# Optimization experiments

Measured on AMD Instinct MI355X. Metric: run time of the kernel, lower is better.

## Reference

```python
import jax, jax.numpy as jnp
import numpy as np

NU, NI, D, E = 200_000, 100_000, 128, 600_000
EPS = 1e-5


def _linear(x, W, b):
    # torch nn.Linear: y = x @ W.T + b, W is [out, in]
    return x @ W.T + b


def _layer_norm(x, g, b):
    mu = jnp.mean(x, axis=-1, keepdims=True)
    var = jnp.mean((x - mu) ** 2, axis=-1, keepdims=True)
    return (x - mu) * jax.lax.rsqrt(var + EPS) * g + b


def _sym_norm_w(row, col, n_src, n_dst):
    ones = jnp.ones(row.shape, jnp.float32)
    deg_s = jax.ops.segment_sum(ones, row, num_segments=n_src)
    deg_d = jax.ops.segment_sum(ones, col, num_segments=n_dst)
    inv_s = jnp.where(deg_s > 0, deg_s ** -0.5, 0.0)
    inv_d = jnp.where(deg_d > 0, deg_d ** -0.5, 0.0)
    return inv_s[row] * inv_d[col]  # [E]


def _relation(x_src, row, col, n_dst, Wl, bl, Wf, bf):
    w = _sym_norm_w(row, col, x_src.shape[0], n_dst)
    m = x_src[row] * w[:, None]                      # gather + scale, [E, D]
    s = jax.ops.segment_sum(m, col, num_segments=n_dst)      # sum messages
    sq = jax.ops.segment_sum(m * m, col, num_segments=n_dst)  # sum of squares
    fm = 0.5 * (s * s - sq)                          # FM interaction
    return _linear(s, Wl, bl) + _linear(fm, Wf, bf)


def setup_inputs() -> dict:
    key = jax.random.key(0)
    ks = jax.random.split(key, 24)
    scale = 1.0 / np.sqrt(D)
    p = lambda k: jax.random.normal(k, (D, D), jnp.float32) * scale
    return {
        "h_user": jax.random.normal(ks[0], (NU, D), jnp.float32),
        "h_item": jax.random.normal(ks[1], (NI, D), jnp.float32),
        "ei_u2i_src": jax.random.randint(ks[2], (E,), 0, NU),
        "ei_u2i_dst": jax.random.randint(ks[3], (E,), 0, NI),
        "ei_i2u_src": jax.random.randint(ks[4], (E,), 0, NI),
        "ei_i2u_dst": jax.random.randint(ks[5], (E,), 0, NU),
        "Ws_user": p(ks[6]), "bs_user": jnp.zeros((D,), jnp.float32),
        "Ws_item": p(ks[7]), "bs_item": jnp.zeros((D,), jnp.float32),
        "Wlin_u2i": p(ks[8]), "blin_u2i": jnp.zeros((D,), jnp.float32),
        "Wfm_u2i": p(ks[9]), "bfm_u2i": jnp.zeros((D,), jnp.float32),
        "Wlin_i2u": p(ks[10]), "blin_i2u": jnp.zeros((D,), jnp.float32),
        "Wfm_i2u": p(ks[11]), "bfm_i2u": jnp.zeros((D,), jnp.float32),
        "g_user": jnp.ones((D,), jnp.float32), "be_user": jnp.zeros((D,), jnp.float32),
        "g_item": jnp.ones((D,), jnp.float32), "be_item": jnp.zeros((D,), jnp.float32),
    }


def reference(h_user, h_item, ei_u2i_src, ei_u2i_dst, ei_i2u_src, ei_i2u_dst,
              Ws_user, bs_user, Ws_item, bs_item,
              Wlin_u2i, blin_u2i, Wfm_u2i, bfm_u2i,
              Wlin_i2u, blin_i2u, Wfm_i2u, bfm_i2u,
              g_user, be_user, g_item, be_item):
    out_u = _linear(h_user, Ws_user, bs_user)
    out_i = _linear(h_item, Ws_item, bs_item)
    # edge type (user, rates, item): src=user, dst=item
    out_i = out_i + _relation(h_user, ei_u2i_src, ei_u2i_dst, NI,
                              Wlin_u2i, blin_u2i, Wfm_u2i, bfm_u2i)
    # edge type (item, rated_by, user): src=item, dst=user
    out_u = out_u + _relation(h_item, ei_i2u_src, ei_i2u_dst, NU,
                              Wlin_i2u, blin_i2u, Wfm_i2u, bfm_i2u)
    out_u = jax.nn.relu(_layer_norm(out_u, g_user, be_user))
    out_i = jax.nn.relu(_layer_norm(out_i, g_item, be_item))
    return out_u, out_i
```

## Files before the change

kernel.cpp:

```cpp
#include <hip/hip_runtime.h>
#include <hip/hip_bf16.h>

#define NU 200000
#define NI 100000
#define DD 128
#define EE 600000
#define CAP 28
#define NXCD 8
#define ZINT (NI + NU + NXCD * NU + NXCD * NI)
#define ZN4 (ZINT / 4)
#define ZB  ((ZN4 + 255) / 256)
#define NW8 (6 * DD * DD / 8)
#define NWB ((NW8 + 255) / 256)
#define NPB2 ((2 * EE + 255) / 256)
#define NIV ((NU + NI + 255) / 256)
#define NSC (((NU + NI) * 16 + 255) / 256)
#define NGAB ((NI + 3) / 4)
#define NGBB ((NU + 3) / 4)
#define NMA ((NI + 127) / 128)
#define NMB ((NU + 127) / 128)

typedef __attribute__((ext_vector_type(8))) short bf16x8;
typedef __attribute__((ext_vector_type(4))) float f32x4;

__device__ __forceinline__ unsigned short f2bf(float f) {
    unsigned int u = __float_as_uint(f);
    u += 0x7fff + ((u >> 16) & 1);
    return (unsigned short)(u >> 16);
}
__device__ __forceinline__ float bf2f(unsigned short h) {
    return __uint_as_float(((unsigned int)h) << 16);
}
__device__ __forceinline__ int xcc_id() {
    unsigned x;
    asm volatile("s_getreg_b32 %0, hwreg(HW_REG_XCC_ID)" : "=s"(x));
    return (int)(x & 7);
}
__device__ __forceinline__ void atomic_inc_l2(int* p) {
    __hip_atomic_fetch_add(p, 1, __ATOMIC_RELAXED, __HIP_MEMORY_SCOPE_WORKGROUP);
}

__global__ void prep_kernel(int* __restrict__ z,
                            const float* __restrict__ w0, const float* __restrict__ w1,
                            const float* __restrict__ w2, const float* __restrict__ w3,
                            const float* __restrict__ w4, const float* __restrict__ w5,
                            unsigned short* __restrict__ wb) {
    int b = blockIdx.x;
    if (b < ZB) {
        int i = b * 256 + threadIdx.x;
        if (i < ZN4) ((int4*)z)[i] = make_int4(0, 0, 0, 0);
        return;
    }
    int i = (b - ZB) * 256 + threadIdx.x;
    if (i >= NW8) return;
    int wsel = i >> 11;
    int k = i & 2047;
    const float* src = (wsel == 0) ? w0 : (wsel == 1) ? w1 : (wsel == 2) ? w2
                     : (wsel == 3) ? w3 : (wsel == 4) ? w4 : w5;
    const float4* p = (const float4*)src + (size_t)k * 2;
    float4 v0 = p[0], v1 = p[1];
    union { unsigned short us[8]; uint4 u4; } r;
    r.us[0] = f2bf(v0.x); r.us[1] = f2bf(v0.y); r.us[2] = f2bf(v0.z); r.us[3] = f2bf(v0.w);
    r.us[4] = f2bf(v1.x); r.us[5] = f2bf(v1.y); r.us[6] = f2bf(v1.z); r.us[7] = f2bf(v1.w);
    ((uint4*)(wb + wsel * DD * DD))[k] = r.u4;
}

__global__ __launch_bounds__(256) void place2_kernel(
        const int* __restrict__ srcA, const int* __restrict__ dstA,
        const int* __restrict__ srcB, const int* __restrict__ dstB,
        int* __restrict__ degAs_p, int* __restrict__ cntA, int* __restrict__ bktA,
        int* __restrict__ degBs_p, int* __restrict__ cntB, int* __restrict__ bktB) {
    int e = blockIdx.x * 256 + threadIdx.x;
    if (e >= 2 * EE) return;
    int xcc = xcc_id();
    if (e < EE) {
        int r = srcA[e], c = dstA[e];
        atomic_inc_l2(&degAs_p[xcc * NU + r]);
        int slot = atomicAdd(&cntA[c], 1);
        if (slot < CAP) bktA[c * CAP + slot] = r;
    } else {
        int f = e - EE;
        int r = srcB[f], c = dstB[f];
        atomic_inc_l2(&degBs_p[xcc * NI + r]);
        int slot = atomicAdd(&cntB[c], 1);
        if (slot < CAP) bktB[c * CAP + slot] = r;
    }
}

__global__ void invmerge_kernel(const int* __restrict__ degAs_p,
                                const int* __restrict__ degBs_p,
                                float* __restrict__ invAs, float* __restrict__ invBs) {
    int i = blockIdx.x * 256 + threadIdx.x;
    if (i < NU) {
        int d = 0;
        #pragma unroll
        for (int x = 0; x < NXCD; ++x) d += degAs_p[x * NU + i];
        invAs[i] = (d > 0) ? rsqrtf((float)d) : 0.f;
    } else if (i < NU + NI) {
        int j = i - NU;
        int d = 0;
        #pragma unroll
        for (int x = 0; x < NXCD; ++x) d += degBs_p[x * NI + j];
        invBs[j] = (d > 0) ? rsqrtf((float)d) : 0.f;
    }
}

__global__ void scaleconv_kernel(const float* __restrict__ h_user,
                                 const float* __restrict__ h_item,
                                 const float* __restrict__ invAs,
                                 const float* __restrict__ invBs,
                                 unsigned short* __restrict__ hubS,
                                 unsigned short* __restrict__ hibS) {
    int i = blockIdx.x * 256 + threadIdx.x;
    const float* h; const float* inv; unsigned short* out; int row, k8;
    if (i < NU * 16) { h = h_user; inv = invAs; out = hubS; row = i >> 4; k8 = (i & 15) * 8; }
    else {
        int j = i - NU * 16;
        if (j >= NI * 16) return;
        h = h_item; inv = invBs; out = hibS; row = j >> 4; k8 = (j & 15) * 8;
    }
    float w = inv[row];
    const float4* p = (const float4*)(h + (size_t)row * DD + k8);
    float4 v0 = p[0], v1 = p[1];
    union { unsigned short us[8]; uint4 u4; } r;
    r.us[0] = f2bf(v0.x * w); r.us[1] = f2bf(v0.y * w);
    r.us[2] = f2bf(v0.z * w); r.us[3] = f2bf(v0.w * w);
    r.us[4] = f2bf(v1.x * w); r.us[5] = f2bf(v1.y * w);
    r.us[6] = f2bf(v1.z * w); r.us[7] = f2bf(v1.w * w);
    *(uint4*)(out + (size_t)row * DD + k8) = r.u4;
}

__device__ __forceinline__ void gather_rows(const unsigned short* __restrict__ xS,
                                            const int* __restrict__ cnt,
                                            const int* __restrict__ bkt,
                                            unsigned short* __restrict__ sOut,
                                            unsigned short* __restrict__ fmOut,
                                            int N, int bid) {
    int d = bid * 4 + (threadIdx.x >> 6);
    int lane = threadIdx.x & 63;
    if (d >= N) return;
    int cfull = cnt[d];
    float invD = (cfull > 0) ? rsqrtf((float)cfull) : 0.f;
    float invD2 = invD * invD;
    int dg = min(cfull, CAP);
    const int* brow = bkt + (size_t)d * CAP;
    float s0 = 0.f, s1 = 0.f, q0 = 0.f, q1 = 0.f;
    for (int j = 0; j < dg; j += 4) {
        int rem = dg - j;
        int4 iv = *(const int4*)(brow + j);
        int i0 = iv.x;
        int i1 = (rem > 1) ? iv.y : i0;
        int i2 = (rem > 2) ? iv.z : i0;
        int i3 = (rem > 3) ? iv.w : i0;
        unsigned int u0 = *(const unsigned int*)(xS + (size_t)i0 * DD + lane * 2);
        unsigned int u1 = *(const unsigned int*)(xS + (size_t)i1 * DD + lane * 2);
        unsigned int u2 = *(const unsigned int*)(xS + (size_t)i2 * DD + lane * 2);
        unsigned int u3 = *(const unsigned int*)(xS + (size_t)i3 * DD + lane * 2);
        u1 = (rem > 1) ? u1 : 0u;
        u2 = (rem > 2) ? u2 : 0u;
        u3 = (rem > 3) ? u3 : 0u;
        float a, b;
        a = bf2f((unsigned short)(u0 & 0xffff)); b = bf2f((unsigned short)(u0 >> 16));
        s0 += a; q0 += a * a; s1 += b; q1 += b * b;
        a = bf2f((unsigned short)(u1 & 0xffff)); b = bf2f((unsigned short)(u1 >> 16));
        s0 += a; q0 += a * a; s1 += b; q1 += b * b;
        a = bf2f((unsigned short)(u2 & 0xffff)); b = bf2f((unsigned short)(u2 >> 16));
        s0 += a; q0 += a * a; s1 += b; q1 += b * b;
        a = bf2f((unsigned short)(u3 & 0xffff)); b = bf2f((unsigned short)(u3 >> 16));
        s0 += a; q0 += a * a; s1 += b; q1 += b * b;
    }
    float ss0 = s0 * invD, ss1 = s1 * invD;
    float f0 = 0.5f * (ss0 * ss0 - q0 * invD2);
    float f1 = 0.5f * (ss1 * ss1 - q1 * invD2);
    unsigned int spack = (unsigned int)f2bf(ss0) | ((unsigned int)f2bf(ss1) << 16);
    unsigned int fpack = (unsigned int)f2bf(f0) | ((unsigned int)f2bf(f1) << 16);
    *(unsigned int*)(sOut  + (size_t)d * DD + lane * 2) = spack;
    *(unsigned int*)(fmOut + (size_t)d * DD + lane * 2) = fpack;
}

__global__ __launch_bounds__(256) void gather2_kernel(
        const unsigned short* __restrict__ hubS, const unsigned short* __restrict__ hibS,
        const int* __restrict__ cntA, const int* __restrict__ bktA,
        const int* __restrict__ cntB, const int* __restrict__ bktB,
        unsigned short* __restrict__ sbA, unsigned short* __restrict__ fbA,
        unsigned short* __restrict__ sbB, unsigned short* __restrict__ fbB) {
    int b = blockIdx.x;
    if (b < NGAB) {
        gather_rows(hubS, cntA, bktA, sbA, fbA, NI, b);
    } else {
        gather_rows(hibS, cntB, bktB, sbB, fbB, NU, b - NGAB);
    }
}

__device__ __forceinline__ bf16x8 a_from_f32(const float* __restrict__ X, size_t off) {
    float4 lo = *(const float4*)(X + off);
    float4 hi = *(const float4*)(X + off + 4);
    union { unsigned short us[8]; bf16x8 v; } r;
    r.us[0] = f2bf(lo.x); r.us[1] = f2bf(lo.y); r.us[2] = f2bf(lo.z); r.us[3] = f2bf(lo.w);
    r.us[4] = f2bf(hi.x); r.us[5] = f2bf(hi.y); r.us[6] = f2bf(hi.z); r.us[7] = f2bf(hi.w);
    return r.v;
}

__device__ __forceinline__ void gemm_ln_block(unsigned char* Wlds, int bid,
        const float* __restrict__ Xh32,
        const unsigned short* __restrict__ Xs, const unsigned short* __restrict__ Xf,
        const unsigned short* __restrict__ W0, const unsigned short* __restrict__ W1,
        const unsigned short* __restrict__ W2,
        const float* __restrict__ B0, const float* __restrict__ B1,
        const float* __restrict__ B2,
        const float* __restrict__ g, const float* __restrict__ be,
        float* __restrict__ out, int N) {
    int tid  = threadIdx.x;
    int wv   = tid >> 6, lane = tid & 63;
    int rlo  = lane & 15, kg = lane >> 4;
    int rowbase = bid * 128 + wv * 32;
    int ar0 = min(rowbase + rlo,      N - 1);
    int ar1 = min(rowbase + 16 + rlo, N - 1);

    f32x4 acc[2][8];
    #pragma unroll
    for (int rt = 0; rt < 2; ++rt)
        #pragma unroll
        for (int jt = 0; jt < 8; ++jt) acc[rt][jt] = (f32x4){0.f, 0.f, 0.f, 0.f};

    const unsigned short* Wp[3] = {W0, W1, W2};
    size_t a0off = (size_t)ar0 * DD + kg * 8;
    size_t a1off = (size_t)ar1 * DD + kg * 8;
    #pragma unroll
    for (int s3 = 0; s3 < 3; ++s3) {
        const uint4* Wg = (const uint4*)Wp[s3];
        #pragma unroll
        for (int it = 0; it < 8; ++it) {
            int slot = it * 256 + tid;
            int row = slot >> 4, c = slot & 15;
            uint4 v = Wg[slot];
            int sc = c ^ (row & 7);
            *(uint4*)(Wlds + ((row << 8) + (sc << 4))) = v;
        }
        __syncthreads();
        #pragma unroll
        for (int ks = 0; ks < 4; ++ks) {
            bf16x8 bfr[8];
            #pragma unroll
            for (int jt = 0; jt < 8; ++jt) {
                int jrow = jt * 16 + rlo;
                int boff = (jrow << 8) + ((((ks << 2) + kg) ^ (jrow & 7)) << 4);
                bfr[jt] = *(const bf16x8*)(Wlds + boff);
            }
            bf16x8 a0, a1;
            if (s3 == 0) {
                a0 = a_from_f32(Xh32, a0off + ks * 32);
                a1 = a_from_f32(Xh32, a1off + ks * 32);
            } else {
                const unsigned short* X = (s3 == 1) ? Xs : Xf;
                a0 = *(const bf16x8*)(X + a0off + ks * 32);
                a1 = *(const bf16x8*)(X + a1off + ks * 32);
            }
            #pragma unroll
            for (int jt = 0; jt < 8; ++jt)
                acc[0][jt] = __builtin_amdgcn_mfma_f32_16x16x32_bf16(a0, bfr[jt], acc[0][jt], 0, 0, 0);
            #pragma unroll
            for (int jt = 0; jt < 8; ++jt)
                acc[1][jt] = __builtin_amdgcn_mfma_f32_16x16x32_bf16(a1, bfr[jt], acc[1][jt], 0, 0, 0);
        }
        __syncthreads();
    }

    float bsum[8], gg[8], bb[8];
    #pragma unroll
    for (int jt = 0; jt < 8; ++jt) {
        int col = jt * 16 + rlo;
        bsum[jt] = B0[col] + B1[col] + B2[col];
        gg[jt] = g[col]; bb[jt] = be[col];
    }
    #pragma unroll
    for (int rt = 0; rt < 2; ++rt) {
        float s1[4] = {0.f, 0.f, 0.f, 0.f}, s2[4] = {0.f, 0.f, 0.f, 0.f};
        #pragma unroll
        for (int jt = 0; jt < 8; ++jt)
            #pragma unroll
            for (int r = 0; r < 4; ++r) {
                float v = acc[rt][jt][r] + bsum[jt];
                acc[rt][jt][r] = v;
                s1[r] += v;
                s2[r] += v * v;
            }
        #pragma unroll
        for (int m = 1; m < 16; m <<= 1)
            #pragma unroll
            for (int r = 0; r < 4; ++r) {
                s1[r] += __shfl_xor(s1[r], m);
                s2[r] += __shfl_xor(s2[r], m);
            }
        #pragma unroll
        for (int r = 0; r < 4; ++r) {
            int grow = rowbase + rt * 16 + kg * 4 + r;
            if (grow >= N) continue;
            float mu  = s1[r] * (1.f / 128.f);
            float var = s2[r] * (1.f / 128.f) - mu * mu;
            float inv = rsqrtf(var + 1e-5f);
            #pragma unroll
            for (int jt = 0; jt < 8; ++jt) {
                int col = jt * 16 + rlo;
                float o = (acc[rt][jt][r] - mu) * inv * gg[jt] + bb[jt];
                out[(size_t)grow * DD + col] = fmaxf(o, 0.f);
            }
        }
    }
}

__global__ __launch_bounds__(256) void gemm2_kernel(
        const float* __restrict__ h_user, const float* __restrict__ h_item,
        const unsigned short* __restrict__ sbA, const unsigned short* __restrict__ fbA,
        const unsigned short* __restrict__ sbB, const unsigned short* __restrict__ fbB,
        const unsigned short* __restrict__ WsU, const unsigned short* __restrict__ WsI,
        const unsigned short* __restrict__ WlA, const unsigned short* __restrict__ WfA,
        const unsigned short* __restrict__ WlB, const unsigned short* __restrict__ WfB,
        const float* __restrict__ bs_user, const float* __restrict__ bs_item,
        const float* __restrict__ blA, const float* __restrict__ bfA,
        const float* __restrict__ blB, const float* __restrict__ bfB,
        const float* __restrict__ g_user, const float* __restrict__ be_user,
        const float* __restrict__ g_item, const float* __restrict__ be_item,
        float* __restrict__ out_u, float* __restrict__ out_i) {
    __shared__ __align__(16) unsigned char Wlds[32768];
    int b = blockIdx.x;
    if (b < NMA) {
        gemm_ln_block(Wlds, b, h_item, sbA, fbA, WsI, WlA, WfA,
                      bs_item, blA, bfA, g_item, be_item, out_i, NI);
    } else {
        gemm_ln_block(Wlds, b - NMA, h_user, sbB, fbB, WsU, WlB, WfB,
                      bs_user, blB, bfB, g_user, be_user, out_u, NU);
    }
}

extern "C" void kernel_launch(void* const* d_in, const int* in_sizes, int n_in,
                              void* d_out, int out_size, void* d_ws, size_t ws_size,
                              hipStream_t stream) {
    const float* h_user   = (const float*)d_in[0];
    const float* h_item   = (const float*)d_in[1];
    const int*   u2i_src  = (const int*)d_in[2];
    const int*   u2i_dst  = (const int*)d_in[3];
    const int*   i2u_src  = (const int*)d_in[4];
    const int*   i2u_dst  = (const int*)d_in[5];
    const float* Ws_user  = (const float*)d_in[6];
    const float* bs_user  = (const float*)d_in[7];
    const float* Ws_item  = (const float*)d_in[8];
    const float* bs_item  = (const float*)d_in[9];
    const float* Wlin_u2i = (const float*)d_in[10];
    const float* blin_u2i = (const float*)d_in[11];
    const float* Wfm_u2i  = (const float*)d_in[12];
    const float* bfm_u2i  = (const float*)d_in[13];
    const float* Wlin_i2u = (const float*)d_in[14];
    const float* blin_i2u = (const float*)d_in[15];
    const float* Wfm_i2u  = (const float*)d_in[16];
    const float* bfm_i2u  = (const float*)d_in[17];
    const float* g_user   = (const float*)d_in[18];
    const float* be_user  = (const float*)d_in[19];
    const float* g_item   = (const float*)d_in[20];
    const float* be_item  = (const float*)d_in[21];

    float* out   = (float*)d_out;
    float* out_u = out;
    float* out_i = out + (size_t)NU * DD;

    char* wsb = (char*)d_ws;
    int* cntA    = (int*)wsb;     wsb += sizeof(int) * NI;
    int* cntB    = (int*)wsb;     wsb += sizeof(int) * NU;
    int* degAs_p = (int*)wsb;     wsb += sizeof(int) * NXCD * NU;
    int* degBs_p = (int*)wsb;     wsb += sizeof(int) * NXCD * NI;
    float* invAs = (float*)wsb;   wsb += sizeof(float) * NU;
    float* invBs = (float*)wsb;   wsb += sizeof(float) * NI;
    int* bktA  = (int*)wsb;       wsb += sizeof(int) * (size_t)NI * CAP;
    int* bktB  = (int*)wsb;       wsb += sizeof(int) * (size_t)NU * CAP;
    unsigned short* hubS = (unsigned short*)wsb;  wsb += sizeof(short) * (size_t)NU * DD;
    unsigned short* hibS = (unsigned short*)wsb;  wsb += sizeof(short) * (size_t)NI * DD;
    unsigned short* sbA = (unsigned short*)wsb;  wsb += sizeof(short) * (size_t)NI * DD;
    unsigned short* fbA = (unsigned short*)wsb;  wsb += sizeof(short) * (size_t)NI * DD;
    unsigned short* sbB = (unsigned short*)wsb;  wsb += sizeof(short) * (size_t)NU * DD;
    unsigned short* fbB = (unsigned short*)wsb;  wsb += sizeof(short) * (size_t)NU * DD;
    unsigned short* wb  = (unsigned short*)wsb;  wsb += sizeof(short) * 6 * DD * DD;
    unsigned short* WsU = wb;
    unsigned short* WsI = wb + 1 * DD * DD;
    unsigned short* WlA = wb + 2 * DD * DD;
    unsigned short* WfA = wb + 3 * DD * DD;
    unsigned short* WlB = wb + 4 * DD * DD;
    unsigned short* WfB = wb + 5 * DD * DD;

    prep_kernel<<<ZB + NWB, 256, 0, stream>>>(
        cntA, Ws_user, Ws_item, Wlin_u2i, Wfm_u2i, Wlin_i2u, Wfm_i2u, wb);

    place2_kernel<<<NPB2, 256, 0, stream>>>(
        u2i_src, u2i_dst, i2u_src, i2u_dst,
        degAs_p, cntA, bktA, degBs_p, cntB, bktB);

    invmerge_kernel<<<NIV, 256, 0, stream>>>(degAs_p, degBs_p, invAs, invBs);

    scaleconv_kernel<<<NSC, 256, 0, stream>>>(h_user, h_item, invAs, invBs, hubS, hibS);

    gather2_kernel<<<NGAB + NGBB, 256, 0, stream>>>(
        hubS, hibS, cntA, bktA, cntB, bktB, sbA, fbA, sbB, fbB);

    gemm2_kernel<<<NMA + NMB, 256, 0, stream>>>(
        h_user, h_item, sbA, fbA, sbB, fbB,
        WsU, WsI, WlA, WfA, WlB, WfB,
        bs_user, bs_item, blin_u2i, bfm_u2i, blin_i2u, bfm_i2u,
        g_user, be_user, g_item, be_item, out_u, out_i);
}
```

Before: 393.6 us.

## Drop per-XCD degree copies and use persistent grid-stride gather

Replaces per-XCC private source-degree counters, which needed workgroup-scope atomics and a merge pass, with single global atomic counters. This shrinks the zero-fill and the inverse-degree pass. The gather kernel becomes a persistent grid-stride loop over 1024 blocks covering both relations, instead of one wave per destination row with one block per 4 rows. The trade is more contention on global atomics in exchange for less memory traffic and fewer block launches.

```diff
diff --git a/kernel.cpp b/kernel.cpp
--- a/kernel.cpp
+++ b/kernel.cpp
@@ -6,8 +6,7 @@
 #define DD 128
 #define EE 600000
 #define CAP 28
-#define NXCD 8
-#define ZINT (NI + NU + NXCD * NU + NXCD * NI)
+#define ZINT (2 * (NU + NI))
 #define ZN4 (ZINT / 4)
 #define ZB  ((ZN4 + 255) / 256)
 #define NW8 (6 * DD * DD / 8)
@@ -15,8 +14,7 @@
 #define NPB2 ((2 * EE + 255) / 256)
 #define NIV ((NU + NI + 255) / 256)
 #define NSC (((NU + NI) * 16 + 255) / 256)
-#define NGAB ((NI + 3) / 4)
-#define NGBB ((NU + 3) / 4)
+#define NGW 1024
 #define NMA ((NI + 127) / 128)
 #define NMB ((NU + 127) / 128)
 
@@ -30,14 +28,6 @@
 }
 __device__ __forceinline__ float bf2f(unsigned short h) {
     return __uint_as_float(((unsigned int)h) << 16);
-}
-__device__ __forceinline__ int xcc_id() {
-    unsigned x;
-    asm volatile("s_getreg_b32 %0, hwreg(HW_REG_XCC_ID)" : "=s"(x));
-    return (int)(x & 7);
-}
-__device__ __forceinline__ void atomic_inc_l2(int* p) {
-    __hip_atomic_fetch_add(p, 1, __ATOMIC_RELAXED, __HIP_MEMORY_SCOPE_WORKGROUP);
 }
 
 __global__ void prep_kernel(int* __restrict__ z,
@@ -65,43 +55,35 @@
     ((uint4*)(wb + wsel * DD * DD))[k] = r.u4;
 }
 
-__global__ __launch_bounds__(256) void place2_kernel(
-        const int* __restrict__ srcA, const int* __restrict__ dstA,
-        const int* __restrict__ srcB, const int* __restrict__ dstB,
-        int* __restrict__ degAs_p, int* __restrict__ cntA, int* __restrict__ bktA,
-        int* __restrict__ degBs_p, int* __restrict__ cntB, int* __restrict__ bktB) {
+__global__ void place2_kernel(const int* __restrict__ srcA, const int* __restrict__ dstA,
+                              const int* __restrict__ srcB, const int* __restrict__ dstB,
+                              int* __restrict__ degAs, int* __restrict__ cntA, int* __restrict__ bktA,
+                              int* __restrict__ degBs, int* __restrict__ cntB, int* __restrict__ bktB) {
     int e = blockIdx.x * 256 + threadIdx.x;
-    if (e >= 2 * EE) return;
-    int xcc = xcc_id();
     if (e < EE) {
         int r = srcA[e], c = dstA[e];
-        atomic_inc_l2(&degAs_p[xcc * NU + r]);
+        atomicAdd(&degAs[r], 1);
         int slot = atomicAdd(&cntA[c], 1);
         if (slot < CAP) bktA[c * CAP + slot] = r;
-    } else {
+    } else if (e < 2 * EE) {
         int f = e - EE;
         int r = srcB[f], c = dstB[f];
-        atomic_inc_l2(&degBs_p[xcc * NI + r]);
+        atomicAdd(&degBs[r], 1);
         int slot = atomicAdd(&cntB[c], 1);
         if (slot < CAP) bktB[c * CAP + slot] = r;
     }
 }
 
-__global__ void invmerge_kernel(const int* __restrict__ degAs_p,
-                                const int* __restrict__ degBs_p,
-                                float* __restrict__ invAs, float* __restrict__ invBs) {
+__global__ void inv2_kernel(const int* __restrict__ degAs, const int* __restrict__ degBs,
+                            float* __restrict__ invAs, float* __restrict__ invBs) {
     int i = blockIdx.x * 256 + threadIdx.x;
     if (i < NU) {
-        int d = 0;
-        #pragma unroll
-        for (int x = 0; x < NXCD; ++x) d += degAs_p[x * NU + i];
-        invAs[i] = (d > 0) ? rsqrtf((float)d) : 0.f;
+        int v = degAs[i];
+        invAs[i] = (v > 0) ? rsqrtf((float)v) : 0.f;
     } else if (i < NU + NI) {
         int j = i - NU;
-        int d = 0;
-        #pragma unroll
-        for (int x = 0; x < NXCD; ++x) d += degBs_p[x * NI + j];
-        invBs[j] = (d > 0) ? rsqrtf((float)d) : 0.f;
+        int v = degBs[j];
+        invBs[j] = (v > 0) ? rsqrtf((float)v) : 0.f;
     }
 }
 
@@ -130,15 +112,12 @@
     *(uint4*)(out + (size_t)row * DD + k8) = r.u4;
 }
 
-__device__ __forceinline__ void gather_rows(const unsigned short* __restrict__ xS,
-                                            const int* __restrict__ cnt,
-                                            const int* __restrict__ bkt,
-                                            unsigned short* __restrict__ sOut,
-                                            unsigned short* __restrict__ fmOut,
-                                            int N, int bid) {
-    int d = bid * 4 + (threadIdx.x >> 6);
-    int lane = threadIdx.x & 63;
-    if (d >= N) return;
+__device__ __forceinline__ void gather_one_row(const unsigned short* __restrict__ xS,
+                                               const int* __restrict__ cnt,
+                                               const int* __restrict__ bkt,
+                                               unsigned short* __restrict__ sOut,
+                                               unsigned short* __restrict__ fmOut,
+                                               int d, int lane) {
     int cfull = cnt[d];
     float invD = (cfull > 0) ? rsqrtf((float)cfull) : 0.f;
     float invD2 = invD * invD;
@@ -184,11 +163,15 @@
         const int* __restrict__ cntB, const int* __restrict__ bktB,
         unsigned short* __restrict__ sbA, unsigned short* __restrict__ fbA,
         unsigned short* __restrict__ sbB, unsigned short* __restrict__ fbB) {
-    int b = blockIdx.x;
-    if (b < NGAB) {
-        gather_rows(hubS, cntA, bktA, sbA, fbA, NI, b);
-    } else {
-        gather_rows(hibS, cntB, bktB, sbB, fbB, NU, b - NGAB);
+    int wid = blockIdx.x * 4 + (threadIdx.x >> 6);
+    int lane = threadIdx.x & 63;
+    const int WTOT = NGW * 4;
+    for (int d = wid; d < NI + NU; d += WTOT) {
+        if (d < NI) {
+            gather_one_row(hubS, cntA, bktA, sbA, fbA, d, lane);
+        } else {
+            gather_one_row(hibS, cntB, bktB, sbB, fbB, d - NI, lane);
+        }
     }
 }
 
@@ -364,10 +347,10 @@
     float* out_i = out + (size_t)NU * DD;
 
     char* wsb = (char*)d_ws;
-    int* cntA    = (int*)wsb;     wsb += sizeof(int) * NI;
-    int* cntB    = (int*)wsb;     wsb += sizeof(int) * NU;
-    int* degAs_p = (int*)wsb;     wsb += sizeof(int) * NXCD * NU;
-    int* degBs_p = (int*)wsb;     wsb += sizeof(int) * NXCD * NI;
+    int* degAs = (int*)wsb;       wsb += sizeof(int) * NU;
+    int* degBs = (int*)wsb;       wsb += sizeof(int) * NI;
+    int* cntA  = (int*)wsb;       wsb += sizeof(int) * NI;
+    int* cntB  = (int*)wsb;       wsb += sizeof(int) * NU;
     float* invAs = (float*)wsb;   wsb += sizeof(float) * NU;
     float* invBs = (float*)wsb;   wsb += sizeof(float) * NI;
     int* bktA  = (int*)wsb;       wsb += sizeof(int) * (size_t)NI * CAP;
@@ -387,17 +370,17 @@
     unsigned short* WfB = wb + 5 * DD * DD;
 
     prep_kernel<<<ZB + NWB, 256, 0, stream>>>(
-        cntA, Ws_user, Ws_item, Wlin_u2i, Wfm_u2i, Wlin_i2u, Wfm_i2u, wb);
+        degAs, Ws_user, Ws_item, Wlin_u2i, Wfm_u2i, Wlin_i2u, Wfm_i2u, wb);
 
     place2_kernel<<<NPB2, 256, 0, stream>>>(
         u2i_src, u2i_dst, i2u_src, i2u_dst,
-        degAs_p, cntA, bktA, degBs_p, cntB, bktB);
-
-    invmerge_kernel<<<NIV, 256, 0, stream>>>(degAs_p, degBs_p, invAs, invBs);
+        degAs, cntA, bktA, degBs, cntB, bktB);
+
+    inv2_kernel<<<NIV, 256, 0, stream>>>(degAs, degBs, invAs, invBs);
 
     scaleconv_kernel<<<NSC, 256, 0, stream>>>(h_user, h_item, invAs, invBs, hubS, hibS);
 
-    gather2_kernel<<<NGAB + NGBB, 256, 0, stream>>>(
+    gather2_kernel<<<NGW, 256, 0, stream>>>(
         hubS, hibS, cntA, bktA, cntB, bktB, sbA, fbA, sbB, fbB);
 
     gemm2_kernel<<<NMA + NMB, 256, 0, stream>>>(
```

Measured after the change: 430.1 us. 9.3% more time.
